# Performance work log

Hardware: AMD Instinct MI355X
Metric: run time of the kernel (lower is better)

## Reference

```python
import jax, jax.numpy as jnp
import numpy as np

F, D = 4, 64          # n_facet, emb_dim
FD = F * D            # cur_dim = 256
NITER = 3             # args.iter

def _embed(x, W, b):
    # SparseInputLinear: torch.mm(x, weight) + bias
    return x @ W + b

def _homo(self_e, neigh_e, a):
    # HomoAttention(emb_dim, n_facet): per-facet gated fusion of self and neighbor embeds
    B = self_e.shape[0]
    s = self_e.reshape(B, F, D)
    n = neigh_e.reshape(B, F, D)
    score = jax.nn.leaky_relu(jnp.concatenate([s, n], axis=-1) @ a, 0.2)  # [B,F]
    alpha = jax.nn.sigmoid(score)[..., None]
    return (s + alpha * n).reshape(B, FD)

def _norm(x):
    return x / (jnp.linalg.norm(x, axis=-1, keepdims=True) + 1e-8)

def _hete(self_e, stacked):
    # HeteAttention(emb_dim, n_facet, niter): disentangled routing over K relation channels
    B, K = stacked.shape[0], stacked.shape[1]
    u0 = _norm(self_e.reshape(B, F, D))
    z = _norm(stacked.reshape(B, K, F, D))
    u = u0
    for _ in range(NITER):
        p = jax.nn.softmax(jnp.einsum('bfd,bkfd->bkf', u, z), axis=1)
        u = _norm(u0 + jnp.einsum('bkf,bkfd->bfd', p, z))
    return u.reshape(B, FD)

def setup_inputs() -> dict:
    key = jax.random.key(0)
    ks = jax.random.split(key, 32)
    B, NU, NB, NC, NG = 1024, 20000, 20000, 1000, 500
    def r(i, shape):
        return jax.random.uniform(ks[i], shape, dtype=jnp.float32)
    def p(i, shape, fan):
        s = 1.0 / np.sqrt(fan)
        return jax.random.uniform(ks[i], shape, minval=-s, maxval=s, dtype=jnp.float32)
    return {
        "users": r(0, (B, NU)), "businesses": r(1, (B, NB)),
        "u_neigh_user": r(2, (B, NU)), "u_neigh_business": r(3, (B, NB)),
        "u_neigh_city": r(4, (B, NC)), "u_neigh_category": r(5, (B, NG)),
        "b_neigh_user": r(6, (B, NU)), "b_neigh_business": r(7, (B, NB)),
        "b_neigh_city": r(8, (B, NC)), "b_neigh_category": r(9, (B, NG)),
        "W_user": p(10, (NU, FD), FD), "b_user": p(11, (FD,), FD),
        "W_bus": p(12, (NB, FD), FD), "b_bus": p(13, (FD,), FD),
        "W_city": p(14, (NC, FD), FD), "b_city": p(15, (FD,), FD),
        "W_cat": p(16, (NG, FD), FD), "b_cat": p(17, (FD,), FD),
        "homo_a": p(18, (8, 2 * D), 2 * D),
    }

def reference(users, businesses, u_neigh_user, u_neigh_business, u_neigh_city, u_neigh_category,
              b_neigh_user, b_neigh_business, b_neigh_city, b_neigh_category,
              W_user, b_user, W_bus, b_bus, W_city, b_city, W_cat, b_cat, homo_a):
    user_embed = _embed(users, W_user, b_user)
    business_embed = _embed(businesses, W_bus, b_bus)
    Ws = [(W_user, b_user), (W_bus, b_bus), (W_city, b_city), (W_cat, b_cat)]
    u_neighs = [u_neigh_user, u_neigh_business, u_neigh_city, u_neigh_category]
    b_neighs = [b_neigh_user, b_neigh_business, b_neigh_city, b_neigh_category]
    u_list = [_homo(user_embed, _embed(n, W, b), homo_a[i])
              for i, (n, (W, b)) in enumerate(zip(u_neighs, Ws))]
    updated_user = _hete(user_embed, jnp.stack(u_list, axis=1))
    b_list = [_homo(business_embed, _embed(n, W, b), homo_a[4 + i])
              for i, (n, (W, b)) in enumerate(zip(b_neighs, Ws))]
    # NOTE: original torch code passes user_embed (not business_embed) as the self
    # node to the business hete encoder; we reproduce that faithfully.
    updated_business = _hete(user_embed, jnp.stack(b_list, axis=1))
    # UserItemAttention / autocross: per-facet interaction logits, softmax over dim=1
    logit = jnp.einsum('bfd,bfd->bf',
                       updated_user.reshape(-1, F, D),
                       updated_business.reshape(-1, F, D))
    return jax.nn.softmax(logit, axis=1)
```

## Files before the change

### kernel.cpp

```cpp
#include <hip/hip_runtime.h>
#include <hip/hip_bf16.h>
#include <stdint.h>
#include <stddef.h>

typedef __attribute__((ext_vector_type(8))) short short8;
typedef __attribute__((ext_vector_type(4))) float f32x4;

#define B_ROWS 1024
#define ND 256
#define MT 128

__device__ __forceinline__ unsigned short f2bf(float x){
  unsigned u = __float_as_uint(x);
  return (unsigned short)((u + 0x7fffu + ((u >> 16) & 1u)) >> 16);
}
__device__ __forceinline__ float bf2f(unsigned short h){
  return __uint_as_float(((unsigned)h) << 16);
}

struct ConvArgs {
  const float* W[4];
  unsigned short* dstHi[4];
  unsigned short* dstLo[4];
  int K[4];
  int chBase[4];
};

__global__ void conv_w_kernel(ConvArgs a){
  int cb = blockIdx.x;
  int w = 0;
  if (cb >= a.chBase[1]) w = 1;
  if (cb >= a.chBase[2]) w = 2;
  if (cb >= a.chBase[3]) w = 3;
  int c = cb - a.chBase[w];
  __shared__ float tile[32][257];
  const float* Wp = a.W[w];
  int K = a.K[w];
  int t = threadIdx.x;
  int r  = t >> 3;
  int c0 = (t & 7) * 32;
  int gk = c * 32 + r;
  if (gk < K){
    const float* src = Wp + (size_t)gk * ND + c0;
    #pragma unroll
    for (int j = 0; j < 32; j += 4){
      float4 v = *(const float4*)(src + j);
      tile[r][c0+j+0] = v.x; tile[r][c0+j+1] = v.y;
      tile[r][c0+j+2] = v.z; tile[r][c0+j+3] = v.w;
    }
  } else {
    #pragma unroll
    for (int j = 0; j < 32; ++j) tile[r][c0+j] = 0.f;
  }
  __syncthreads();
  int n = t;
  unsigned short hi[32], lo[32];
  #pragma unroll
  for (int k = 0; k < 32; ++k){
    float x = tile[k][n];
    unsigned short h = f2bf(x);
    hi[k] = h;
    lo[k] = f2bf(x - bf2f(h));
  }
  size_t base = ((size_t)c * ND + n) * 32;
  unsigned short* dh = a.dstHi[w] + base;
  unsigned short* dl = a.dstLo[w] + base;
  union { unsigned short u[8]; uint4 v; } pk;
  #pragma unroll
  for (int q = 0; q < 4; ++q){
    #pragma unroll
    for (int e = 0; e < 8; ++e) pk.u[e] = hi[q*8+e];
    *(uint4*)(dh + q*8) = pk.v;
    #pragma unroll
    for (int e = 0; e < 8; ++e) pk.u[e] = lo[q*8+e];
    *(uint4*)(dl + q*8) = pk.v;
  }
}

struct BiasArgs { float* emb; const float* b[10]; };

__global__ void bias_init_kernel(BiasArgs a){
  int idx = blockIdx.x * blockDim.x + threadIdx.x;
  int g  = idx >> 16;
  int wi = idx & 65535;
  int n4 = (wi & 63) * 4;
  const float* bp = a.b[g];
  float4 v; v.x = bp[n4]; v.y = bp[n4+1]; v.z = bp[n4+2]; v.w = bp[n4+3];
  *(float4*)(a.emb + (size_t)idx * 4) = v;
}

struct GemmArgs {
  const float* X[10];
  const unsigned short* Wh[10];
  const unsigned short* Wl[10];
  float* C[10];
  int K[10];
  int nch[10];
  int ksplit[10];
  int wgBase[11];
};

__launch_bounds__(256, 2)
__global__ void gemm_kernel(GemmArgs a){
  __shared__ unsigned short Ah[MT][40];
  __shared__ unsigned short Al[MT][40];

  int bid = blockIdx.x;
  int g = 0;
  while (bid >= a.wgBase[g+1]) ++g;
  int loc = bid - a.wgBase[g];
  int mt = loc & 7;
  int ks = loc >> 3;
  int nch = a.nch[g];
  int ksp = a.ksplit[g];
  int q = nch / ksp, r = nch % ksp;
  int c0  = ks * q + (ks < r ? ks : r);
  int cnt = q + (ks < r ? 1 : 0);

  const float* X = a.X[g];
  int K = a.K[g];
  const unsigned short* Wh = a.Wh[g];
  const unsigned short* Wl = a.Wl[g];

  int t = threadIdx.x;
  int lane = t & 63, w = t >> 6;
  int ln15 = lane & 15, kg = lane >> 4;
  int rowbase = mt * MT;
  int srow = t >> 1, sseg = (t & 1) * 16;
  const float* xrow = X + (size_t)(rowbase + srow) * K;

  f32x4 acc[8][4];
  #pragma unroll
  for (int i = 0; i < 8; ++i)
    #pragma unroll
    for (int j = 0; j < 4; ++j) acc[i][j] = (f32x4){0.f,0.f,0.f,0.f};

  for (int ci = 0; ci < cnt; ++ci){
    int c = c0 + ci;
    short8 bh[4], bl[4];
    size_t cb = (size_t)c * (ND * 32);
    #pragma unroll
    for (int j = 0; j < 4; ++j){
      size_t offs = cb + (size_t)(w*64 + j*16 + ln15) * 32 + kg*8;
      bh[j] = *(const short8*)(Wh + offs);
      bl[j] = *(const short8*)(Wl + offs);
    }
    int gk0 = c * 32 + sseg;
    float xv[16];
    if (gk0 + 16 <= K){
      #pragma unroll
      for (int j = 0; j < 16; j += 4){
        float4 v = *(const float4*)(xrow + gk0 + j);
        xv[j] = v.x; xv[j+1] = v.y; xv[j+2] = v.z; xv[j+3] = v.w;
      }
    } else {
      #pragma unroll
      for (int j = 0; j < 16; ++j) xv[j] = (gk0 + j < K) ? xrow[gk0 + j] : 0.f;
    }
    unsigned short hh[16], ll[16];
    #pragma unroll
    for (int j = 0; j < 16; ++j){
      unsigned short h = f2bf(xv[j]);
      hh[j] = h;
      ll[j] = f2bf(xv[j] - bf2f(h));
    }
    __syncthreads();
    union { unsigned short u[8]; uint4 v; } pk;
    #pragma unroll
    for (int q2 = 0; q2 < 2; ++q2){
      #pragma unroll
      for (int e = 0; e < 8; ++e) pk.u[e] = hh[q2*8+e];
      *(uint4*)&Ah[srow][sseg + q2*8] = pk.v;
      #pragma unroll
      for (int e = 0; e < 8; ++e) pk.u[e] = ll[q2*8+e];
      *(uint4*)&Al[srow][sseg + q2*8] = pk.v;
    }
    __syncthreads();
    #pragma unroll
    for (int i = 0; i < 8; ++i){
      const short8 ah = *(const short8*)&Ah[i*16 + ln15][kg*8];
      const short8 al = *(const short8*)&Al[i*16 + ln15][kg*8];
      #pragma unroll
      for (int j = 0; j < 4; ++j){
        acc[i][j] = __builtin_amdgcn_mfma_f32_16x16x32_bf16(ah, bh[j], acc[i][j], 0, 0, 0);
        acc[i][j] = __builtin_amdgcn_mfma_f32_16x16x32_bf16(ah, bl[j], acc[i][j], 0, 0, 0);
        acc[i][j] = __builtin_amdgcn_mfma_f32_16x16x32_bf16(al, bh[j], acc[i][j], 0, 0, 0);
      }
    }
  }
  float* C = a.C[g];
  int crow0 = (lane >> 4) * 4;
  #pragma unroll
  for (int i = 0; i < 8; ++i){
    #pragma unroll
    for (int j = 0; j < 4; ++j){
      int col = w*64 + j*16 + ln15;
      #pragma unroll
      for (int rr = 0; rr < 4; ++rr){
        int row = rowbase + i*16 + crow0 + rr;
        atomicAdd(&C[(size_t)row * ND + col], acc[i][j][rr]);
      }
    }
  }
}

__device__ __forceinline__ float wsum(float v){
  #pragma unroll
  for (int m = 32; m; m >>= 1) v += __shfl_xor(v, m, 64);
  return v;
}

__global__ void fuse_kernel(const float* __restrict__ emb,
                            const float* __restrict__ homo_a,
                            float* __restrict__ out){
  int b = blockIdx.x;
  int t = threadIdx.x;
  int f = t >> 6;
  int d = t & 63;
  auto E = [&](int g){ return emb[((size_t)g * B_ROWS + b) * ND + t]; };

  float us = E(0), bs = E(1);
  float un[4], bn[4];
  #pragma unroll
  for (int i = 0; i < 4; ++i){ un[i] = E(2+i); bn[i] = E(6+i); }

  float ul[4], blv[4];
  #pragma unroll
  for (int i = 0; i < 4; ++i){
    float as_ = homo_a[i*128 + d],     an_ = homo_a[i*128 + 64 + d];
    float sc  = wsum(us*as_ + un[i]*an_);
    sc = sc > 0.f ? sc : 0.2f*sc;
    float alp = 1.f / (1.f + expf(-sc));
    ul[i] = us + alp*un[i];
    float as2 = homo_a[(4+i)*128 + d], an2 = homo_a[(4+i)*128 + 64 + d];
    float sc2 = wsum(bs*as2 + bn[i]*an2);
    sc2 = sc2 > 0.f ? sc2 : 0.2f*sc2;
    float alp2 = 1.f / (1.f + expf(-sc2));
    blv[i] = bs + alp2*bn[i];
  }

  float u0 = us / (sqrtf(wsum(us*us)) + 1e-8f);
  float zu[4], zb[4];
  #pragma unroll
  for (int i = 0; i < 4; ++i){
    zu[i] = ul[i]  / (sqrtf(wsum(ul[i]*ul[i]))   + 1e-8f);
    zb[i] = blv[i] / (sqrtf(wsum(blv[i]*blv[i])) + 1e-8f);
  }

  auto route = [&](float z0, float z1, float z2, float z3)->float{
    float u = u0;
    #pragma unroll
    for (int it = 0; it < 3; ++it){
      float d0 = wsum(u*z0), d1 = wsum(u*z1), d2 = wsum(u*z2), d3 = wsum(u*z3);
      float m = fmaxf(fmaxf(d0,d1), fmaxf(d2,d3));
      float e0 = expf(d0-m), e1 = expf(d1-m), e2 = expf(d2-m), e3 = expf(d3-m);
      float s = e0+e1+e2+e3;
      float nu = u0 + (e0*z0 + e1*z1 + e2*z2 + e3*z3) / s;
      u = nu / (sqrtf(wsum(nu*nu)) + 1e-8f);
    }
    return u;
  };

  float uu = route(zu[0], zu[1], zu[2], zu[3]);
  float ub = route(zb[0], zb[1], zb[2], zb[3]);

  float lg = wsum(uu*ub);
  __shared__ float sl[4];
  if (d == 0) sl[f] = lg;
  __syncthreads();
  if (t < 4){
    float l0 = sl[0], l1 = sl[1], l2 = sl[2], l3 = sl[3];
    float m = fmaxf(fmaxf(l0,l1), fmaxf(l2,l3));
    float den = expf(l0-m) + expf(l1-m) + expf(l2-m) + expf(l3-m);
    out[(size_t)b*4 + t] = expf(sl[t]-m) / den;
  }
}

extern "C" void kernel_launch(void* const* d_in, const int* in_sizes, int n_in,
                              void* d_out, int out_size, void* d_ws, size_t ws_size,
                              hipStream_t stream) {
  const float* X[10];
  for (int i = 0; i < 10; ++i) X[i] = (const float*)d_in[i];
  const float* Wm[4]   = { (const float*)d_in[10], (const float*)d_in[12],
                           (const float*)d_in[14], (const float*)d_in[16] };
  const float* bias[4] = { (const float*)d_in[11], (const float*)d_in[13],
                           (const float*)d_in[15], (const float*)d_in[17] };
  const float* homo_a  = (const float*)d_in[18];
  float* out = (float*)d_out;

  const size_t EMB_FLOATS = 10ull * B_ROWS * ND;
  float* emb = (float*)d_ws;
  unsigned short* wch = (unsigned short*)((char*)d_ws + EMB_FLOATS * 4);
  const int nchW[4] = {625, 625, 32, 16};
  size_t off[8];
  {
    size_t o = 0;
    for (int w = 0; w < 4; ++w){
      off[2*w]   = o; o += (size_t)nchW[w] * ND * 32;
      off[2*w+1] = o; o += (size_t)nchW[w] * ND * 32;
    }
  }
  const int Kw[4] = {20000, 20000, 1000, 500};

  ConvArgs ca;
  int cbase = 0;
  for (int w = 0; w < 4; ++w){
    ca.W[w] = Wm[w];
    ca.dstHi[w] = wch + off[2*w];
    ca.dstLo[w] = wch + off[2*w+1];
    ca.K[w] = Kw[w];
    ca.chBase[w] = cbase;
    cbase += nchW[w];
  }
  hipLaunchKernelGGL(conv_w_kernel, dim3(cbase), dim3(256), 0, stream, ca);

  static const int biasOf[10] = {0,1,0,1,2,3,0,1,2,3};
  BiasArgs ba;
  ba.emb = emb;
  for (int g = 0; g < 10; ++g) ba.b[g] = bias[biasOf[g]];
  hipLaunchKernelGGL(bias_init_kernel, dim3((EMB_FLOATS/4)/256), dim3(256), 0, stream, ba);

  static const int wOf[10]  = {0,1,0,1,2,3,0,1,2,3};
  static const int ksp[10]  = {10,10,10,10,2,1,10,10,2,1};
  GemmArgs ga;
  int base = 0;
  for (int g = 0; g < 10; ++g){
    ga.X[g]  = X[g];
    ga.Wh[g] = wch + off[2*wOf[g]];
    ga.Wl[g] = wch + off[2*wOf[g]+1];
    ga.C[g]  = emb + (size_t)g * B_ROWS * ND;
    ga.K[g]  = Kw[wOf[g]];
    ga.nch[g] = nchW[wOf[g]];
    ga.ksplit[g] = ksp[g];
    ga.wgBase[g] = base;
    base += 8 * ksp[g];
  }
  ga.wgBase[10] = base;
  hipLaunchKernelGGL(gemm_kernel, dim3(base), dim3(256), 0, stream, ga);

  hipLaunchKernelGGL(fuse_kernel, dim3(B_ROWS), dim3(256), 0, stream, emb, homo_a, out);
}
```

Baseline: 597.5 us.

## Switch GEMM to fp16 with split-X only, smaller M tiles and X prefetch

Weights are now stored as a single fp16 copy instead of a bf16 hi/lo pair. X is split into fp16 hi+lo terms, so each tile needs two MFMAs instead of three. The M tile shrinks from 128 to 64 rows, which doubles the block count. Occupancy is raised to 3 blocks, blocks are swizzled across groups, and X rows are register-prefetched two chunks ahead. The aim is to halve weight traffic and MFMA work and to better hide global load latency, at the cost of dropping weight precision to single fp16 and a risk of fp16 range/accuracy issues.

```diff
diff --git a/kernel.cpp b/kernel.cpp
--- a/kernel.cpp
+++ b/kernel.cpp
@@ -3,25 +3,15 @@
 #include <stdint.h>
 #include <stddef.h>
 
-typedef __attribute__((ext_vector_type(8))) short short8;
+typedef __attribute__((ext_vector_type(8))) _Float16 f16x8;
 typedef __attribute__((ext_vector_type(4))) float f32x4;
 
 #define B_ROWS 1024
 #define ND 256
-#define MT 128
-
-__device__ __forceinline__ unsigned short f2bf(float x){
-  unsigned u = __float_as_uint(x);
-  return (unsigned short)((u + 0x7fffu + ((u >> 16) & 1u)) >> 16);
-}
-__device__ __forceinline__ float bf2f(unsigned short h){
-  return __uint_as_float(((unsigned)h) << 16);
-}
 
 struct ConvArgs {
   const float* W[4];
-  unsigned short* dstHi[4];
-  unsigned short* dstLo[4];
+  unsigned short* dst[4];
   int K[4];
   int chBase[4];
 };
@@ -37,8 +27,7 @@
   const float* Wp = a.W[w];
   int K = a.K[w];
   int t = threadIdx.x;
-  int r  = t >> 3;
-  int c0 = (t & 7) * 32;
+  int r = t >> 3, c0 = (t & 7) * 32;
   int gk = c * 32 + r;
   if (gk < K){
     const float* src = Wp + (size_t)gk * ND + c0;
@@ -54,27 +43,15 @@
   }
   __syncthreads();
   int n = t;
-  unsigned short hi[32], lo[32];
+  union { unsigned short s[32]; uint4 v[4]; } pk;
   #pragma unroll
   for (int k = 0; k < 32; ++k){
-    float x = tile[k][n];
-    unsigned short h = f2bf(x);
-    hi[k] = h;
-    lo[k] = f2bf(x - bf2f(h));
-  }
-  size_t base = ((size_t)c * ND + n) * 32;
-  unsigned short* dh = a.dstHi[w] + base;
-  unsigned short* dl = a.dstLo[w] + base;
-  union { unsigned short u[8]; uint4 v; } pk;
-  #pragma unroll
-  for (int q = 0; q < 4; ++q){
-    #pragma unroll
-    for (int e = 0; e < 8; ++e) pk.u[e] = hi[q*8+e];
-    *(uint4*)(dh + q*8) = pk.v;
-    #pragma unroll
-    for (int e = 0; e < 8; ++e) pk.u[e] = lo[q*8+e];
-    *(uint4*)(dl + q*8) = pk.v;
-  }
+    _Float16 h = (_Float16)tile[k][n];
+    pk.s[k] = *(unsigned short*)&h;
+  }
+  unsigned short* d = a.dst[w] + ((size_t)c * ND + n) * 32;
+  #pragma unroll
+  for (int q = 0; q < 4; ++q) *(uint4*)(d + q*8) = pk.v[q];
 }
 
 struct BiasArgs { float* emb; const float* b[10]; };
@@ -92,7 +69,6 @@
 struct GemmArgs {
   const float* X[10];
   const unsigned short* Wh[10];
-  const unsigned short* Wl[10];
   float* C[10];
   int K[10];
   int nch[10];
@@ -100,19 +76,32 @@
   int wgBase[11];
 };
 
-__launch_bounds__(256, 2)
+__device__ __forceinline__ void load8(float* d, const float* p, int k0, int K){
+  if (k0 + 8 <= K){
+    float4 v0 = *(const float4*)(p + k0);
+    float4 v1 = *(const float4*)(p + k0 + 4);
+    d[0]=v0.x; d[1]=v0.y; d[2]=v0.z; d[3]=v0.w;
+    d[4]=v1.x; d[5]=v1.y; d[6]=v1.z; d[7]=v1.w;
+  } else {
+    #pragma unroll
+    for (int j = 0; j < 8; ++j) d[j] = (k0 + j < K) ? p[k0 + j] : 0.f;
+  }
+}
+
+__launch_bounds__(256, 3)
 __global__ void gemm_kernel(GemmArgs a){
-  __shared__ unsigned short Ah[MT][40];
-  __shared__ unsigned short Al[MT][40];
-
-  int bid = blockIdx.x;
+  __shared__ _Float16 Ah[64][40];
+  __shared__ _Float16 Al[64][40];
+
+  int nx = (int)gridDim.x >> 3;
+  int bid = ((int)blockIdx.x & 7) * nx + ((int)blockIdx.x >> 3);
+
   int g = 0;
   while (bid >= a.wgBase[g+1]) ++g;
   int loc = bid - a.wgBase[g];
-  int mt = loc & 7;
-  int ks = loc >> 3;
-  int nch = a.nch[g];
-  int ksp = a.ksplit[g];
+  int mt = loc & 15;
+  int ks = loc >> 4;
+  int nch = a.nch[g], ksp = a.ksplit[g];
   int q = nch / ksp, r = nch % ksp;
   int c0  = ks * q + (ks < r ? ks : r);
   int cnt = q + (ks < r ? 1 : 0);
@@ -120,78 +109,66 @@
   const float* X = a.X[g];
   int K = a.K[g];
   const unsigned short* Wh = a.Wh[g];
-  const unsigned short* Wl = a.Wl[g];
 
   int t = threadIdx.x;
   int lane = t & 63, w = t >> 6;
   int ln15 = lane & 15, kg = lane >> 4;
-  int rowbase = mt * MT;
-  int srow = t >> 1, sseg = (t & 1) * 16;
+  int rowbase = mt * 64;
+  int srow = t >> 2, sk = (t & 3) * 8;
   const float* xrow = X + (size_t)(rowbase + srow) * K;
 
-  f32x4 acc[8][4];
-  #pragma unroll
-  for (int i = 0; i < 8; ++i)
+  f32x4 acc[4][4];
+  #pragma unroll
+  for (int i = 0; i < 4; ++i)
     #pragma unroll
     for (int j = 0; j < 4; ++j) acc[i][j] = (f32x4){0.f,0.f,0.f,0.f};
+
+  float cur[8], nx1[8];
+  load8(cur, xrow, c0*32 + sk, K);
+  if (cnt > 1) load8(nx1, xrow, (c0+1)*32 + sk, K);
 
   for (int ci = 0; ci < cnt; ++ci){
     int c = c0 + ci;
-    short8 bh[4], bl[4];
+    f16x8 bh[4];
     size_t cb = (size_t)c * (ND * 32);
     #pragma unroll
-    for (int j = 0; j < 4; ++j){
-      size_t offs = cb + (size_t)(w*64 + j*16 + ln15) * 32 + kg*8;
-      bh[j] = *(const short8*)(Wh + offs);
-      bl[j] = *(const short8*)(Wl + offs);
-    }
-    int gk0 = c * 32 + sseg;
-    float xv[16];
-    if (gk0 + 16 <= K){
-      #pragma unroll
-      for (int j = 0; j < 16; j += 4){
-        float4 v = *(const float4*)(xrow + gk0 + j);
-        xv[j] = v.x; xv[j+1] = v.y; xv[j+2] = v.z; xv[j+3] = v.w;
-      }
+    for (int j = 0; j < 4; ++j)
+      bh[j] = *(const f16x8*)(Wh + cb + (size_t)(w*64 + j*16 + ln15) * 32 + kg*8);
+    float nx2[8];
+    if (ci + 2 < cnt){
+      load8(nx2, xrow, (c+2)*32 + sk, K);
     } else {
-      #pragma unroll
-      for (int j = 0; j < 16; ++j) xv[j] = (gk0 + j < K) ? xrow[gk0 + j] : 0.f;
-    }
-    unsigned short hh[16], ll[16];
-    #pragma unroll
-    for (int j = 0; j < 16; ++j){
-      unsigned short h = f2bf(xv[j]);
-      hh[j] = h;
-      ll[j] = f2bf(xv[j] - bf2f(h));
+      for (int j = 0; j < 8; ++j) nx2[j] = 0.f;
+    }
+    union { _Float16 h[8]; uint4 u; } H, L;
+    #pragma unroll
+    for (int j = 0; j < 8; ++j){
+      _Float16 h = (_Float16)cur[j];
+      H.h[j] = h;
+      L.h[j] = (_Float16)(cur[j] - (float)h);
     }
     __syncthreads();
-    union { unsigned short u[8]; uint4 v; } pk;
-    #pragma unroll
-    for (int q2 = 0; q2 < 2; ++q2){
-      #pragma unroll
-      for (int e = 0; e < 8; ++e) pk.u[e] = hh[q2*8+e];
-      *(uint4*)&Ah[srow][sseg + q2*8] = pk.v;
-      #pragma unroll
-      for (int e = 0; e < 8; ++e) pk.u[e] = ll[q2*8+e];
-      *(uint4*)&Al[srow][sseg + q2*8] = pk.v;
-    }
+    *(uint4*)&Ah[srow][sk] = H.u;
+    *(uint4*)&Al[srow][sk] = L.u;
     __syncthreads();
     #pragma unroll
-    for (int i = 0; i < 8; ++i){
-      const short8 ah = *(const short8*)&Ah[i*16 + ln15][kg*8];
-      const short8 al = *(const short8*)&Al[i*16 + ln15][kg*8];
+    for (int i = 0; i < 4; ++i){
+      f16x8 ah = *(const f16x8*)&Ah[i*16 + ln15][kg*8];
+      f16x8 al = *(const f16x8*)&Al[i*16 + ln15][kg*8];
       #pragma unroll
       for (int j = 0; j < 4; ++j){
-        acc[i][j] = __builtin_amdgcn_mfma_f32_16x16x32_bf16(ah, bh[j], acc[i][j], 0, 0, 0);
-        acc[i][j] = __builtin_amdgcn_mfma_f32_16x16x32_bf16(ah, bl[j], acc[i][j], 0, 0, 0);
-        acc[i][j] = __builtin_amdgcn_mfma_f32_16x16x32_bf16(al, bh[j], acc[i][j], 0, 0, 0);
+        acc[i][j] = __builtin_amdgcn_mfma_f32_16x16x32_f16(ah, bh[j], acc[i][j], 0, 0, 0);
+        acc[i][j] = __builtin_amdgcn_mfma_f32_16x16x32_f16(al, bh[j], acc[i][j], 0, 0, 0);
       }
     }
-  }
+    #pragma unroll
+    for (int j = 0; j < 8; ++j){ cur[j] = nx1[j]; nx1[j] = nx2[j]; }
+  }
+
   float* C = a.C[g];
-  int crow0 = (lane >> 4) * 4;
-  #pragma unroll
-  for (int i = 0; i < 8; ++i){
+  int crow0 = kg * 4;
+  #pragma unroll
+  for (int i = 0; i < 4; ++i){
     #pragma unroll
     for (int j = 0; j < 4; ++j){
       int col = w*64 + j*16 + ln15;
@@ -292,22 +269,18 @@
   float* emb = (float*)d_ws;
   unsigned short* wch = (unsigned short*)((char*)d_ws + EMB_FLOATS * 4);
   const int nchW[4] = {625, 625, 32, 16};
-  size_t off[8];
+  const int Kw[4]   = {20000, 20000, 1000, 500};
+  size_t off[4];
   {
     size_t o = 0;
-    for (int w = 0; w < 4; ++w){
-      off[2*w]   = o; o += (size_t)nchW[w] * ND * 32;
-      off[2*w+1] = o; o += (size_t)nchW[w] * ND * 32;
-    }
-  }
-  const int Kw[4] = {20000, 20000, 1000, 500};
+    for (int w = 0; w < 4; ++w){ off[w] = o; o += (size_t)nchW[w] * ND * 32; }
+  }
 
   ConvArgs ca;
   int cbase = 0;
   for (int w = 0; w < 4; ++w){
     ca.W[w] = Wm[w];
-    ca.dstHi[w] = wch + off[2*w];
-    ca.dstLo[w] = wch + off[2*w+1];
+    ca.dst[w] = wch + off[w];
     ca.K[w] = Kw[w];
     ca.chBase[w] = cbase;
     cbase += nchW[w];
@@ -320,20 +293,19 @@
   for (int g = 0; g < 10; ++g) ba.b[g] = bias[biasOf[g]];
   hipLaunchKernelGGL(bias_init_kernel, dim3((EMB_FLOATS/4)/256), dim3(256), 0, stream, ba);
 
-  static const int wOf[10]  = {0,1,0,1,2,3,0,1,2,3};
-  static const int ksp[10]  = {10,10,10,10,2,1,10,10,2,1};
+  static const int wOf[10] = {0,1,0,1,2,3,0,1,2,3};
+  static const int ksp[10] = {10,10,10,10,2,1,10,10,2,1};
   GemmArgs ga;
   int base = 0;
   for (int g = 0; g < 10; ++g){
     ga.X[g]  = X[g];
-    ga.Wh[g] = wch + off[2*wOf[g]];
-    ga.Wl[g] = wch + off[2*wOf[g]+1];
+    ga.Wh[g] = wch + off[wOf[g]];
     ga.C[g]  = emb + (size_t)g * B_ROWS * ND;
     ga.K[g]  = Kw[wOf[g]];
     ga.nch[g] = nchW[wOf[g]];
     ga.ksplit[g] = ksp[g];
     ga.wgBase[g] = base;
-    base += 8 * ksp[g];
+    base += 16 * ksp[g];
   }
   ga.wgBase[10] = base;
   hipLaunchKernelGGL(gemm_kernel, dim3(base), dim3(256), 0, stream, ga);
```

New measurement: 601.3 us. No clear change (+0.6%).
